# Performance work log

Measured on AMD Instinct MI355X. Metric: run time of the kernel, lower is better.

The kernel has to match this reference:

```python
import jax, jax.numpy as jnp
import numpy as np

N = 4096      # mesh nodes (seq len)
D = 512       # input_dim_nodes / hidden_size
F = 512       # ffn_hidden_size (hidden_dim)
NH = 4        # num_attention_heads
HD = D // NH  # head dim = 128
L = 2         # processor_layers
EPS = 1e-5
SCALE = 1.0 / float(np.sqrt(HD))
NEG = -1e9


def setup_inputs() -> dict:
    key = jax.random.key(0)
    ks = jax.random.split(key, 16)
    nfeat = jax.random.normal(ks[0], (N, D), jnp.float32)
    # sparse graph adjacency mask: True = masked out (TE 'arbitrary' convention)
    mask = jax.random.uniform(ks[1], (N, N)) < 0.99
    idx = jnp.arange(N)
    mask = mask.at[idx, idx].set(False)  # keep self-edges unmasked
    s = 0.02
    p = lambda k, shape: jax.random.normal(k, shape, jnp.float32) * s
    return dict(
        nfeat=nfeat, mask=mask,
        ln1_g=jnp.ones((L, D), jnp.float32), ln1_b=jnp.zeros((L, D), jnp.float32),
        wq=p(ks[2], (L, D, D)), bq=p(ks[3], (L, D)),
        wk=p(ks[4], (L, D, D)), bk=p(ks[5], (L, D)),
        wv=p(ks[6], (L, D, D)), bv=p(ks[7], (L, D)),
        wo=p(ks[8], (L, D, D)), bo=p(ks[9], (L, D)),
        ln2_g=jnp.ones((L, D), jnp.float32), ln2_b=jnp.zeros((L, D), jnp.float32),
        fc1_w=p(ks[10], (L, F, D)), fc1_b=p(ks[11], (L, F)),
        fc2_w=p(ks[12], (L, D, F)), fc2_b=p(ks[13], (L, D)),
    )


def _ln(x, g, b):
    mu = x.mean(-1, keepdims=True)
    var = ((x - mu) ** 2).mean(-1, keepdims=True)
    return (x - mu) * jax.lax.rsqrt(var + EPS) * g + b


def reference(nfeat, mask, ln1_g, ln1_b, wq, bq, wk, bk, wv, bv, wo, bo,
              ln2_g, ln2_b, fc1_w, fc1_b, fc2_w, fc2_b):
    def layer(x, p):
        g1, b1, Wq, Bq, Wk, Bk, Wv, Bv, Wo, Bo, g2, b2, W1, B1, W2, B2 = p
        # --- pre-LN self-attention with arbitrary mask ---
        h = _ln(x, g1, b1)                                  # [N, D]
        q = (h @ Wq.T + Bq).reshape(N, NH, HD)
        k = (h @ Wk.T + Bk).reshape(N, NH, HD)
        v = (h @ Wv.T + Bv).reshape(N, NH, HD)
        scores = jnp.einsum('qhd,khd->hqk', q, k) * SCALE   # [NH, N, N]
        scores = jnp.where(mask[None], NEG, scores)
        attn = jax.nn.softmax(scores, axis=-1)
        o = jnp.einsum('hqk,khd->qhd', attn, v).reshape(N, D)
        x = x + o @ Wo.T + Bo
        # --- pre-LN MLP ---
        h2 = _ln(x, g2, b2)
        m = jax.nn.gelu(h2 @ W1.T + B1, approximate=False) @ W2.T + B2
        return x + m, None

    xs = (ln1_g, ln1_b, wq, bq, wk, bk, wv, bv, wo, bo,
          ln2_g, ln2_b, fc1_w, fc1_b, fc2_w, fc2_b)
    out, _ = jax.lax.scan(layer, nfeat, xs)
    return out
```

## Files before the change

### kernel.cpp

```cpp
#include <hip/hip_runtime.h>
#include <math.h>

#define NN 4096
#define DD 512
#define FF 512
#define CAP 256
#define SCALE 0.08838834764831845f

typedef unsigned short u16;
typedef unsigned char u8;
typedef unsigned int u32;
typedef __attribute__((ext_vector_type(8))) short short8;
typedef __attribute__((ext_vector_type(8))) unsigned short ushort8;
typedef __attribute__((ext_vector_type(4))) unsigned short ushort4v;
typedef __attribute__((ext_vector_type(4))) float floatx4;
typedef __attribute__((ext_vector_type(2))) float f32x2;
typedef _Float16 half8v __attribute__((ext_vector_type(8)));

__device__ __forceinline__ u16 f2bf(float f) {
    union { float f; unsigned int i; } x; x.f = f;
    unsigned int r = (x.i + 0x7FFFu + ((x.i >> 16) & 1u)) >> 16;
    return (u16)r;
}
__device__ __forceinline__ u16 f2h(float f) {
    _Float16 h = (_Float16)f;
    union { _Float16 h; u16 u; } x; x.h = h; return x.u;
}
__device__ __forceinline__ u8 f2fp8(float f) {
    union { _Float16 h; u16 u; } x;
    x.h = (_Float16)(f * 0.00390625f);
    u16 h = x.u;
    h = h + 0x3F + ((h >> 7) & 1);
    return (u8)(((h >> 8) & 0x80) | ((h >> 7) & 0x7f));
}
__device__ __forceinline__ float fp82f_sw(u8 b) {
    union { u16 u; _Float16 h; } x;
    x.u = (u16)(((u16)(b & 0x80) << 8) | ((u16)(b & 0x7f) << 7));
    return (float)x.h * 256.0f;
}
__device__ __forceinline__ void gld_lds16(const void* g, void* l) {
    __builtin_amdgcn_global_load_lds((const __attribute__((address_space(1))) void*)g,
                                     (__attribute__((address_space(3))) void*)l, 16, 0, 0);
}

__device__ __forceinline__ float gelu_fast(float val) {
    float z = fabsf(val) * 0.70710678118654752f;
    float tt = __builtin_amdgcn_rcpf(fmaf(0.3275911f, z, 1.0f));
    float p = fmaf(1.061405429f, tt, -1.453152027f);
    p = fmaf(p, tt, 1.421413741f);
    p = fmaf(p, tt, -0.284496736f);
    p = fmaf(p, tt, 0.254829592f);
    p = p * tt * __expf(-z * z);
    float er_ = 1.0f - p;
    float sgn = (val < 0.f) ? -er_ : er_;
    return val * 0.5f * (1.0f + sgn);
}

struct SP {
    const float* w[6];
    const float* bq; const float* bk; const float* bv; const float* fc1_b;
    const float* ln1_g; const float* ln1_b; const float* ln2_g; const float* ln2_b;
    const float* nfeat; const int* mask;
};
__global__ void setup_kernel(SP sp, u16* __restrict__ wc, float* __restrict__ bc2,
                             float* __restrict__ c1c, float* __restrict__ st,
                             u16* __restrict__ xb, int* __restrict__ idx,
                             int* __restrict__ cnt) {
    const int bid = blockIdx.x;
    const int t = threadIdx.x;
    const int wave = t >> 6, lane = t & 63;
    if (bid < 192) {
        int region = bid >> 4;
        int layer = region / 6, mat = region - layer * 6;
        const float* src = sp.w[mat] + (size_t)layer * (DD * DD);
        u16* d = wc + (size_t)region * (DD * DD);
        int off = (bid & 15) * 16384 + t * 4;
        int k = (t * 4) & 511;
        float4 g4 = {1.f, 1.f, 1.f, 1.f};
        if (mat < 3)      g4 = *(const float4*)&sp.ln1_g[layer * DD + k];
        else if (mat == 4) g4 = *(const float4*)&sp.ln2_g[layer * DD + k];
#pragma unroll
        for (int i = 0; i < 16; i++) {
            int e = off + i * 1024;
            float4 f = *(const float4*)&src[e];
            ushort4v u;
            u.x = f2bf(f.x * g4.x); u.y = f2bf(f.y * g4.y);
            u.z = f2bf(f.z * g4.z); u.w = f2bf(f.w * g4.w);
            *(ushort4v*)&d[e] = u;
        }
        if (bid == 2 || bid == 3) {
            float* z = st + 8192;
            int base = (bid - 2) * 256 + t;
#pragma unroll
            for (int i = 0; i < 48; i++) z[base + i * 512] = 0.0f;
        }
        return;
    }
    if (bid < 192 + NN) {
        int row = bid - 192;
        __shared__ int c;
        __shared__ float ws[4][2];
        const float* xr = sp.nfeat + (size_t)row * DD;
        float2 v2 = *(const float2*)&xr[t * 2];
        float s1 = v2.x + v2.y, s2 = v2.x * v2.x + v2.y * v2.y;
#pragma unroll
        for (int off = 32; off; off >>= 1) { s1 += __shfl_xor(s1, off); s2 += __shfl_xor(s2, off); }
        if (lane == 0) { ws[wave][0] = s1; ws[wave][1] = s2; }
        u32 pack = (u32)f2bf(v2.x) | ((u32)f2bf(v2.y) << 16);
        ((u32*)xb)[row * 256 + t] = pack;
        if (t == 0) c = 0;
        __syncthreads();
        if (t == 0) {
            float S1 = ws[0][0] + ws[1][0] + ws[2][0] + ws[3][0];
            float S2 = ws[0][1] + ws[1][1] + ws[2][1] + ws[3][1];
            st[row * 2] = S1; st[row * 2 + 1] = S2;
        }
        const int4* mrow = (const int4*)(sp.mask + (size_t)row * NN);
        for (int j4 = t; j4 < NN / 4; j4 += blockDim.x) {
            int4 m4 = mrow[j4];
            int base = j4 * 4;
            if (m4.x == 0) idx[row * CAP + atomicAdd(&c, 1)] = base;
            if (m4.y == 0) idx[row * CAP + atomicAdd(&c, 1)] = base + 1;
            if (m4.z == 0) idx[row * CAP + atomicAdd(&c, 1)] = base + 2;
            if (m4.w == 0) idx[row * CAP + atomicAdd(&c, 1)] = base + 3;
        }
        __syncthreads();
        if (t == 0) cnt[row] = (c < CAP) ? c : CAP;
        return;
    }
    {
        int colg = (bid - (192 + NN)) * 4 + wave;
        int l = colg >> 11, j = colg & 2047;
        const float* W; const float* g; const float* b; float bias;
        if (j < 1536) {
            int mat = j >> 9, col = j & 511;
            W = sp.w[mat] + (size_t)l * DD * DD + (size_t)col * DD;
            g = sp.ln1_g + l * DD; b = sp.ln1_b + l * DD;
            bias = (mat == 0 ? sp.bq : mat == 1 ? sp.bk : sp.bv)[l * DD + col];
        } else {
            int col = j - 1536;
            W = sp.w[4] + (size_t)l * DD * DD + (size_t)col * DD;
            g = sp.ln2_g + l * DD; b = sp.ln2_b + l * DD;
            bias = sp.fc1_b[l * DD + col];
        }
        int k = lane * 8;
        float4 w0 = *(const float4*)&W[k];
        float4 w1 = *(const float4*)&W[k + 4];
        float4 g0 = *(const float4*)&g[k];
        float4 g1 = *(const float4*)&g[k + 4];
        float4 b0 = *(const float4*)&b[k];
        float4 b1 = *(const float4*)&b[k + 4];
        float c1 = w0.x * g0.x + w0.y * g0.y + w0.z * g0.z + w0.w * g0.w
                 + w1.x * g1.x + w1.y * g1.y + w1.z * g1.z + w1.w * g1.w;
        float c2 = w0.x * b0.x + w0.y * b0.y + w0.z * b0.z + w0.w * b0.w
                 + w1.x * b1.x + w1.y * b1.y + w1.z * b1.z + w1.w * b1.w;
#pragma unroll
        for (int off = 32; off; off >>= 1) { c1 += __shfl_xor(c1, off); c2 += __shfl_xor(c2, off); }
        if (lane == 0) { c1c[colg] = c1; bc2[colg] = bias + c2; }
    }
}


template <int MODE, int LNF>
__launch_bounds__(256)
__global__ void gemm_fc(const u16* __restrict__ A, const u16* __restrict__ B,
                        const float* __restrict__ bias, const float* __restrict__ c1,
                        const float* __restrict__ stats, const float* __restrict__ resIn,
                        float* __restrict__ resOut, u16* __restrict__ outB,
                        u16* __restrict__ xbOut, float* __restrict__ statsOut) {
    __shared__ __align__(16) u8 smem[16384];
    u16* As = (u16*)smem;
    u16* Bs = (u16*)(smem + 8192);
    const int m0 = blockIdx.y * 64, n0 = blockIdx.x * 64;
    const int t = threadIdx.x;
    const int wave = t >> 6, lane = t & 63;
    const int wm = (wave & 1) * 32, wn = (wave >> 1) * 32;
    const int sr = t >> 3;
    const int sc = ((((t & 7) - (t >> 3)) & 7)) * 8;
    const int fr = lane & 15, g0 = lane >> 4;
    const int er = (lane >> 4) * 4, ec = lane & 15;

    floatx4 acc[2][2] = {};
    const u16* ag0 = A + (size_t)(m0 + sr) * 512 + sc;
    const u16* ag1 = A + (size_t)(m0 + 32 + sr) * 512 + sc;
    const u16* bg0 = B + (size_t)(n0 + sr) * 512 + sc;
    const u16* bg1 = B + (size_t)(n0 + 32 + sr) * 512 + sc;

    float rin[16];
    if (MODE == 2) {
#pragma unroll
        for (int i = 0; i < 2; i++)
#pragma unroll
            for (int j = 0; j < 2; j++)
#pragma unroll
                for (int r = 0; r < 4; r++)
                    rin[(i * 2 + j) * 4 + r] =
                        resIn[(size_t)(m0 + wm + 16 * i + er + r) * 512 + (n0 + wn + 16 * j + ec)];
    }
    float ar[2][4], br[2][4];
    if (LNF) {
#pragma unroll
        for (int i = 0; i < 2; i++) {
            int r0 = m0 + wm + 16 * i + er;
#pragma unroll
            for (int r = 0; r < 4; r++) {
                f32x2 s = *(const f32x2*)&stats[(r0 + r) * 2];
                float m = s.x * (1.0f / DD);
                float rr = rsqrtf(s.y * (1.0f / DD) - m * m + 1e-5f);
                ar[i][r] = rr; br[i][r] = -rr * m;
            }
        }
    }

    for (int k0 = 0; k0 < 512; k0 += 64) {
        __syncthreads();
        gld_lds16(ag0 + k0, As + t * 8);
        gld_lds16(ag1 + k0, As + 2048 + t * 8);
        gld_lds16(bg0 + k0, Bs + t * 8);
        gld_lds16(bg1 + k0, Bs + 2048 + t * 8);
        __syncthreads();
#pragma unroll
        for (int h = 0; h < 2; h++) {
            const int fo = (((h << 2) + g0 + fr) & 7) << 3;
            short8 af[2], bf[2];
#pragma unroll
            for (int i = 0; i < 2; i++) af[i] = *(const short8*)&As[(wm + 16 * i + fr) * 64 + fo];
#pragma unroll
            for (int j = 0; j < 2; j++) bf[j] = *(const short8*)&Bs[(wn + 16 * j + fr) * 64 + fo];
#pragma unroll
            for (int i = 0; i < 2; i++)
#pragma unroll
                for (int j = 0; j < 2; j++)
                    acc[i][j] = __builtin_amdgcn_mfma_f32_16x16x32_bf16(af[i], bf[j], acc[i][j], 0, 0, 0);
        }
    }

    float outv[16];
#pragma unroll
    for (int j = 0; j < 2; j++) {
        int col = n0 + wn + 16 * j + ec;
        float bsv = bias[col];
        float c1v = LNF ? c1[col] : 0.f;
#pragma unroll
        for (int i = 0; i < 2; i++) {
#pragma unroll
            for (int r = 0; r < 4; r++) {
                int row = m0 + wm + 16 * i + er + r;
                float val;
                if (LNF) val = fmaf(ar[i][r], acc[i][j][r], fmaf(br[i][r], c1v, bsv));
                else     val = acc[i][j][r] + bsv;
                if (MODE == 1) {
                    outB[(size_t)row * 512 + col] = f2bf(gelu_fast(val));
                } else {
                    float ov = rin[(i * 2 + j) * 4 + r] + val;
                    outv[(i * 2 + j) * 4 + r] = ov;
                    resOut[(size_t)row * 512 + col] = ov;
                    if (xbOut) xbOut[(size_t)row * 512 + col] = f2bf(ov);
                }
            }
        }
    }

    if (MODE == 2 && statsOut) {
        __syncthreads();
        float* Ls = (float*)smem;
#pragma unroll
        for (int i = 0; i < 2; i++)
#pragma unroll
            for (int j = 0; j < 2; j++)
#pragma unroll
                for (int r = 0; r < 4; r++)
                    Ls[(wm + 16 * i + er + r) * 64 + (wn + 16 * j + ec)] = outv[(i * 2 + j) * 4 + r];
        __syncthreads();
        if (t < 64) {
            float s1 = 0.f, s2 = 0.f;
            for (int c0 = 0; c0 < 64; c0++) {
                int cc = (c0 + t) & 63;
                float v = Ls[t * 64 + cc];
                s1 += v; s2 += v * v;
            }
            atomicAdd(&statsOut[(size_t)(m0 + t) * 2], s1);
            atomicAdd(&statsOut[(size_t)(m0 + t) * 2 + 1], s2);
        }
    }
}

__launch_bounds__(256)
__global__ void gemm_qkv(const u16* __restrict__ A, const u16* __restrict__ B,
                         const float* __restrict__ bias, const float* __restrict__ c1,
                         const float* __restrict__ stats, u16* __restrict__ qOut,
                         u8* __restrict__ kv8) {
    __shared__ u16 As[128 * 64];
    __shared__ u16 Bs[64 * 64];
    const int m0 = blockIdx.y * 128, n0 = blockIdx.x * 64;
    const int t = threadIdx.x;
    const int wave = t >> 6, lane = t & 63;
    const int wm = (wave & 1) * 64, wn = (wave >> 1) * 32;
    const int sr = t >> 3;
    const int sc = ((((t & 7) - (t >> 3)) & 7)) * 8;
    const int fr = lane & 15, g0 = lane >> 4;
    const int er = (lane >> 4) * 4, ec = lane & 15;

    floatx4 acc[4][2] = {};
    const u16* agp[4];
    u16* asp[4];
#pragma unroll
    for (int u = 0; u < 4; u++) {
        agp[u] = A + (size_t)(m0 + 32 * u + sr) * DD + sc;
        asp[u] = As + u * (32 * 64) + t * 8;
    }
    const u16* bg0 = B + (size_t)(n0 + sr) * DD + sc;
    const u16* bg1 = B + (size_t)(n0 + 32 + sr) * DD + sc;

    float ar[4][4], br[4][4];
#pragma unroll
    for (int i = 0; i < 4; i++) {
        int r0 = m0 + wm + 16 * i + er;
#pragma unroll
        for (int r = 0; r < 4; r++) {
            f32x2 s = *(const f32x2*)&stats[(r0 + r) * 2];
            float m = s.x * (1.0f / DD);
            float rr = rsqrtf(s.y * (1.0f / DD) - m * m + 1e-5f);
            ar[i][r] = rr; br[i][r] = -rr * m;
        }
    }

    for (int k0 = 0; k0 < DD; k0 += 64) {
        __syncthreads();
#pragma unroll
        for (int u = 0; u < 4; u++) gld_lds16(agp[u] + k0, asp[u]);
        gld_lds16(bg0 + k0, Bs + t * 8);
        gld_lds16(bg1 + k0, Bs + 2048 + t * 8);
        __syncthreads();
#pragma unroll
        for (int h = 0; h < 2; h++) {
            const int fo = (((h << 2) + g0 + fr) & 7) << 3;
            short8 af[4], bf[2];
#pragma unroll
            for (int i = 0; i < 4; i++) af[i] = *(const short8*)&As[(wm + 16 * i + fr) * 64 + fo];
#pragma unroll
            for (int j = 0; j < 2; j++) bf[j] = *(const short8*)&Bs[(wn + 16 * j + fr) * 64 + fo];
#pragma unroll
            for (int i = 0; i < 4; i++)
#pragma unroll
                for (int j = 0; j < 2; j++)
                    acc[i][j] = __builtin_amdgcn_mfma_f32_16x16x32_bf16(af[i], bf[j], acc[i][j], 0, 0, 0);
        }
    }

    const int bx = blockIdx.x;
#pragma unroll
    for (int j = 0; j < 2; j++) {
        int col = n0 + wn + 16 * j + ec;
        float bsv = bias[col];
        float c1v = c1[col];
#pragma unroll
        for (int i = 0; i < 4; i++) {
#pragma unroll
            for (int r = 0; r < 4; r++) {
                int row = m0 + wm + 16 * i + er + r;
                float val = fmaf(ar[i][r], acc[i][j][r], fmaf(br[i][r], c1v, bsv));
                if (bx < 8) {
                    qOut[(size_t)row * 512 + col] = f2h(val);
                } else if (bx < 16) {
                    int cc = col - 512;
                    kv8[(size_t)row * 1024 + 16 * (cc >> 3) + (cc & 7)] = f2fp8(val);
                } else {
                    int cc = col - 1024;
                    kv8[(size_t)row * 1024 + 16 * (cc >> 3) + 8 + (cc & 7)] = f2fp8(val);
                }
            }
        }
    }
}

__global__ void sparse_attn(const u16* __restrict__ q, const u8* __restrict__ kv8,
                            const int* __restrict__ idx, const int* __restrict__ cnt,
                            u16* __restrict__ o) {
    int t = threadIdx.x;
    int wave = t >> 6, lane = t & 63;
    int qslot = wave >> 1, half = wave & 1;
    int qi = blockIdx.x * 4 + qslot;
    __shared__ float obuf[4][64][8];
    __shared__ float sbuf[4][64];
    __shared__ int sidx[4][CAP];

    int c = cnt[qi];
    const int* ir = idx + qi * CAP;
    for (int j = t & 127; j < c; j += 128) sidx[qslot][j] = ir[j];

    half8v qv = *(const half8v*)(q + (size_t)qi * 512 + lane * 8);
    float qf[8];
#pragma unroll
    for (int e = 0; e < 8; e++) qf[e] = (float)qv[e];
    __syncthreads();

    float sum = 0.f, oa[8] = {};
    int j = half;
    int4 kv0, kv1;
    {
        int k0i = (j < c) ? sidx[qslot][j] : 0;
        int k1i = (j + 2 < c) ? sidx[qslot][j + 2] : 0;
        kv0 = *(const int4*)(kv8 + (size_t)k0i * 1024 + lane * 16);
        kv1 = *(const int4*)(kv8 + (size_t)k1i * 1024 + lane * 16);
    }
    while (j < c) {
        int4 kvn;
        {
            int kjn = (j + 4 < c) ? sidx[qslot][j + 4] : 0;
            kvn = *(const int4*)(kv8 + (size_t)kjn * 1024 + lane * 16);
        }
        float kd[8], vd[8];
#if __has_builtin(__builtin_amdgcn_cvt_pk_f32_fp8)
        {
            f32x2 p0 = __builtin_amdgcn_cvt_pk_f32_fp8(kv0.x, false);
            f32x2 p1 = __builtin_amdgcn_cvt_pk_f32_fp8(kv0.x, true);
            f32x2 p2 = __builtin_amdgcn_cvt_pk_f32_fp8(kv0.y, false);
            f32x2 p3 = __builtin_amdgcn_cvt_pk_f32_fp8(kv0.y, true);
            kd[0] = p0.x; kd[1] = p0.y; kd[2] = p1.x; kd[3] = p1.y;
            kd[4] = p2.x; kd[5] = p2.y; kd[6] = p3.x; kd[7] = p3.y;
            f32x2 p4 = __builtin_amdgcn_cvt_pk_f32_fp8(kv0.z, false);
            f32x2 p5 = __builtin_amdgcn_cvt_pk_f32_fp8(kv0.z, true);
            f32x2 p6 = __builtin_amdgcn_cvt_pk_f32_fp8(kv0.w, false);
            f32x2 p7 = __builtin_amdgcn_cvt_pk_f32_fp8(kv0.w, true);
            vd[0] = p4.x; vd[1] = p4.y; vd[2] = p5.x; vd[3] = p5.y;
            vd[4] = p6.x; vd[5] = p6.y; vd[6] = p7.x; vd[7] = p7.y;
        }
#else
        {
            const u8* bp = (const u8*)&kv0;
#pragma unroll
            for (int e = 0; e < 8; e++) { kd[e] = fp82f_sw(bp[e]); vd[e] = fp82f_sw(bp[8 + e]); }
        }
#endif
        float d = 0.f;
#pragma unroll
        for (int e = 0; e < 8; e++) d = fmaf(qf[e], kd[e], d);
        d += __shfl_xor(d, 1);
        d += __shfl_xor(d, 2);
        d += __shfl_xor(d, 4);
        d += __shfl_xor(d, 8);
        float p = __expf(d * SCALE);
        sum += p;
#pragma unroll
        for (int e = 0; e < 8; e++) oa[e] = fmaf(p, vd[e], oa[e]);
        kv0 = kv1;
        kv1 = kvn;
        j += 2;
    }

    if (half == 1) {
#pragma unroll
        for (int e = 0; e < 8; e++) obuf[qslot][lane][e] = oa[e];
        sbuf[qslot][lane] = sum;
    }
    __syncthreads();
    if (half == 0) {
        sum += sbuf[qslot][lane];
        float inv = 1.0f / sum;
        ushort8 ov;
#pragma unroll
        for (int e = 0; e < 8; e++) ov[e] = f2bf((oa[e] + obuf[qslot][lane][e]) * inv);
        *(ushort8*)(o + (size_t)qi * 512 + lane * 8) = ov;
    }
}

extern "C" void kernel_launch(void* const* d_in, const int* in_sizes, int n_in,
                              void* d_out, int out_size, void* d_ws, size_t ws_size,
                              hipStream_t stream) {
    const float* nfeat = (const float*)d_in[0];
    const float* bo    = (const float*)d_in[11];
    const float* fc2_b = (const float*)d_in[17];

    const size_t ND = (size_t)NN * DD;
    const size_t SS = (size_t)DD * DD;
    float* x    = (float*)d_ws;
    u16*   xb   = (u16*)(x + ND);
    u16*   q    = xb + ND;
    u8*    kv8  = (u8*)(q + ND);
    u16*   o    = (u16*)(kv8 + (size_t)NN * 1024);
    u16*   m1   = o + ND;
    u16*   wc   = m1 + ND;
    float* bc2  = (float*)(wc + 12 * SS);
    float* c1c  = bc2 + 2 * 2048;
    float* st   = c1c + 2 * 2048;
    int*   idx  = (int*)(st + 4 * 8192);
    int*   cnt  = idx + (size_t)NN * CAP;

    SP sp;
    sp.w[0] = (const float*)d_in[4];  sp.bq = (const float*)d_in[5];
    sp.w[1] = (const float*)d_in[6];  sp.bk = (const float*)d_in[7];
    sp.w[2] = (const float*)d_in[8];  sp.bv = (const float*)d_in[9];
    sp.w[3] = (const float*)d_in[10];
    sp.w[4] = (const float*)d_in[14]; sp.fc1_b = (const float*)d_in[15];
    sp.w[5] = (const float*)d_in[16];
    sp.ln1_g = (const float*)d_in[2];  sp.ln1_b = (const float*)d_in[3];
    sp.ln2_g = (const float*)d_in[12]; sp.ln2_b = (const float*)d_in[13];
    sp.nfeat = nfeat; sp.mask = (const int*)d_in[1];

    setup_kernel<<<192 + NN + 1024, 256, 0, stream>>>(sp, wc, bc2, c1c, st, xb, idx, cnt);

    for (int l = 0; l < 2; l++) {
        size_t bOff = (size_t)l * DD;
        u16* wl = wc + (size_t)l * 6 * SS;
        const float* xin = (l == 0) ? nfeat : x;
        float* fc2_dst = (l == 1) ? (float*)d_out : x;
        float* st_ln1 = st + (l == 0 ? 0 : 2) * 8192;
        float* st_ln2 = st + (l == 0 ? 1 : 3) * 8192;

        gemm_qkv<<<dim3(24, 32), 256, 0, stream>>>(xb, wl, bc2 + l * 2048, c1c + l * 2048,
                                                   st_ln1, q, kv8);
        sparse_attn<<<NN / 4, 512, 0, stream>>>(q, kv8, idx, cnt, o);
        gemm_fc<2, 0><<<dim3(8, 64), 256, 0, stream>>>(o, wl + 3 * SS, bo + bOff, nullptr,
                                                       nullptr, xin, x, nullptr, xb, st_ln2);
        gemm_fc<1, 1><<<dim3(8, 64), 256, 0, stream>>>(xb, wl + 4 * SS,
                                                       bc2 + l * 2048 + 1536,
                                                       c1c + l * 2048 + 1536,
                                                       st_ln2, nullptr, nullptr, m1,
                                                       nullptr, nullptr);
        gemm_fc<2, 0><<<dim3(8, 64), 256, 0, stream>>>(m1, wl + 5 * SS, fc2_b + bOff, nullptr,
                                                       nullptr, x, fc2_dst, nullptr,
                                                       (l == 0) ? xb : nullptr,
                                                       (l == 0) ? (st + 2 * 8192) : nullptr);
    }
}
```

Before: 272.7 us.

## Move mask compaction into layer-0 QKV GEMM using wave ballot prefix sums

The sparse-mask index compaction leaves the setup kernel and runs in extra blocks appended to the layer-0 QKV GEMM grid, so the mask scan overlaps with the GEMM work. Each wave now compacts one row in order using ballot and popcount instead of shared-memory atomics. This also yields deterministic, sorted neighbour lists. The setup kernel's per-row LN statistics and bf16 conversion are reshaped to one row per wave, which cuts the setup grid. The cost is a larger QKV launch with heterogeneous blocks, and the mask read (64 MB of int32) still dominates and now sits on the QKV kernel's critical path.

```diff
diff --git a/kernel.cpp b/kernel.cpp
--- a/kernel.cpp
+++ b/kernel.cpp
@@ -60,12 +60,11 @@
     const float* w[6];
     const float* bq; const float* bk; const float* bv; const float* fc1_b;
     const float* ln1_g; const float* ln1_b; const float* ln2_g; const float* ln2_b;
-    const float* nfeat; const int* mask;
+    const float* nfeat;
 };
 __global__ void setup_kernel(SP sp, u16* __restrict__ wc, float* __restrict__ bc2,
                              float* __restrict__ c1c, float* __restrict__ st,
-                             u16* __restrict__ xb, int* __restrict__ idx,
-                             int* __restrict__ cnt) {
+                             u16* __restrict__ xb) {
     const int bid = blockIdx.x;
     const int t = threadIdx.x;
     const int wave = t >> 6, lane = t & 63;
@@ -96,40 +95,26 @@
         }
         return;
     }
-    if (bid < 192 + NN) {
-        int row = bid - 192;
-        __shared__ int c;
-        __shared__ float ws[4][2];
-        const float* xr = sp.nfeat + (size_t)row * DD;
-        float2 v2 = *(const float2*)&xr[t * 2];
-        float s1 = v2.x + v2.y, s2 = v2.x * v2.x + v2.y * v2.y;
+    if (bid < 192 + 1024) {
+        int row = (bid - 192) * 4 + wave;
+        const float* xr = sp.nfeat + (size_t)row * DD + lane * 8;
+        float4 a = *(const float4*)xr;
+        float4 b4 = *(const float4*)(xr + 4);
+        float v[8] = {a.x, a.y, a.z, a.w, b4.x, b4.y, b4.z, b4.w};
+        float s1 = 0.f, s2 = 0.f;
+#pragma unroll
+        for (int e = 0; e < 8; e++) { s1 += v[e]; s2 += v[e] * v[e]; }
 #pragma unroll
         for (int off = 32; off; off >>= 1) { s1 += __shfl_xor(s1, off); s2 += __shfl_xor(s2, off); }
-        if (lane == 0) { ws[wave][0] = s1; ws[wave][1] = s2; }
-        u32 pack = (u32)f2bf(v2.x) | ((u32)f2bf(v2.y) << 16);
-        ((u32*)xb)[row * 256 + t] = pack;
-        if (t == 0) c = 0;
-        __syncthreads();
-        if (t == 0) {
-            float S1 = ws[0][0] + ws[1][0] + ws[2][0] + ws[3][0];
-            float S2 = ws[0][1] + ws[1][1] + ws[2][1] + ws[3][1];
-            st[row * 2] = S1; st[row * 2 + 1] = S2;
-        }
-        const int4* mrow = (const int4*)(sp.mask + (size_t)row * NN);
-        for (int j4 = t; j4 < NN / 4; j4 += blockDim.x) {
-            int4 m4 = mrow[j4];
-            int base = j4 * 4;
-            if (m4.x == 0) idx[row * CAP + atomicAdd(&c, 1)] = base;
-            if (m4.y == 0) idx[row * CAP + atomicAdd(&c, 1)] = base + 1;
-            if (m4.z == 0) idx[row * CAP + atomicAdd(&c, 1)] = base + 2;
-            if (m4.w == 0) idx[row * CAP + atomicAdd(&c, 1)] = base + 3;
-        }
-        __syncthreads();
-        if (t == 0) cnt[row] = (c < CAP) ? c : CAP;
+        if (lane == 0) { st[row * 2] = s1; st[row * 2 + 1] = s2; }
+        ushort8 ov;
+#pragma unroll
+        for (int e = 0; e < 8; e++) ov[e] = f2bf(v[e]);
+        *(ushort8*)&xb[(size_t)row * DD + lane * 8] = ov;
         return;
     }
     {
-        int colg = (bid - (192 + NN)) * 4 + wave;
+        int colg = (bid - (192 + 1024)) * 4 + wave;
         int l = colg >> 11, j = colg & 2047;
         const float* W; const float* g; const float* b; float bias;
         if (j < 1536) {
@@ -285,16 +270,44 @@
     }
 }
 
+template <int DOMASK>
 __launch_bounds__(256)
 __global__ void gemm_qkv(const u16* __restrict__ A, const u16* __restrict__ B,
                          const float* __restrict__ bias, const float* __restrict__ c1,
                          const float* __restrict__ stats, u16* __restrict__ qOut,
-                         u8* __restrict__ kv8) {
+                         u8* __restrict__ kv8, const int* __restrict__ mask,
+                         int* __restrict__ idx, int* __restrict__ cnt) {
     __shared__ u16 As[128 * 64];
     __shared__ u16 Bs[64 * 64];
-    const int m0 = blockIdx.y * 128, n0 = blockIdx.x * 64;
     const int t = threadIdx.x;
     const int wave = t >> 6, lane = t & 63;
+
+    if (DOMASK && blockIdx.y >= 32) {
+        int mb = (blockIdx.y - 32) * 24 + blockIdx.x;
+        int row = mb * 4 + wave;
+        if (row < NN) {
+            const int4* mrow = (const int4*)(mask + (size_t)row * NN);
+            int base = 0;
+#pragma unroll 4
+            for (int it = 0; it < 16; it++) {
+                int4 m4 = mrow[it * 64 + lane];
+                int cbase = (it * 64 + lane) * 4;
+                int mv[4] = {m4.x, m4.y, m4.z, m4.w};
+#pragma unroll
+                for (int cmp = 0; cmp < 4; cmp++) {
+                    unsigned long long bl = __ballot(mv[cmp] == 0);
+                    int pre = __popcll(bl & ((1ull << lane) - 1ull));
+                    int pos = base + pre;
+                    if (mv[cmp] == 0 && pos < CAP) idx[row * CAP + pos] = cbase + cmp;
+                    base += __popcll(bl);
+                }
+            }
+            if (lane == 0) cnt[row] = (base < CAP) ? base : CAP;
+        }
+        return;
+    }
+
+    const int m0 = blockIdx.y * 128, n0 = blockIdx.x * 64;
     const int wm = (wave & 1) * 64, wn = (wave >> 1) * 32;
     const int sr = t >> 3;
     const int sc = ((((t & 7) - (t >> 3)) & 7)) * 8;
@@ -469,6 +482,7 @@
                               void* d_out, int out_size, void* d_ws, size_t ws_size,
                               hipStream_t stream) {
     const float* nfeat = (const float*)d_in[0];
+    const int*   mask  = (const int*)d_in[1];
     const float* bo    = (const float*)d_in[11];
     const float* fc2_b = (const float*)d_in[17];
 
@@ -496,9 +510,9 @@
     sp.w[5] = (const float*)d_in[16];
     sp.ln1_g = (const float*)d_in[2];  sp.ln1_b = (const float*)d_in[3];
     sp.ln2_g = (const float*)d_in[12]; sp.ln2_b = (const float*)d_in[13];
-    sp.nfeat = nfeat; sp.mask = (const int*)d_in[1];
-
-    setup_kernel<<<192 + NN + 1024, 256, 0, stream>>>(sp, wc, bc2, c1c, st, xb, idx, cnt);
+    sp.nfeat = nfeat;
+
+    setup_kernel<<<192 + 1024 + 1024, 256, 0, stream>>>(sp, wc, bc2, c1c, st, xb);
 
     for (int l = 0; l < 2; l++) {
         size_t bOff = (size_t)l * DD;
@@ -508,8 +522,13 @@
         float* st_ln1 = st + (l == 0 ? 0 : 2) * 8192;
         float* st_ln2 = st + (l == 0 ? 1 : 3) * 8192;
 
-        gemm_qkv<<<dim3(24, 32), 256, 0, stream>>>(xb, wl, bc2 + l * 2048, c1c + l * 2048,
-                                                   st_ln1, q, kv8);
+        if (l == 0) {
+            gemm_qkv<1><<<dim3(24, 32 + 43), 256, 0, stream>>>(xb, wl, bc2, c1c,
+                                                               st_ln1, q, kv8, mask, idx, cnt);
+        } else {
+            gemm_qkv<0><<<dim3(24, 32), 256, 0, stream>>>(xb, wl, bc2 + 2048, c1c + 2048,
+                                                          st_ln1, q, kv8, nullptr, idx, cnt);
+        }
         sparse_attn<<<NN / 4, 512, 0, stream>>>(q, kv8, idx, cnt, o);
         gemm_fc<2, 0><<<dim3(8, 64), 256, 0, stream>>>(o, wl + 3 * SS, bo + bOff, nullptr,
                                                        nullptr, xin, x, nullptr, xb, st_ln2);
```

Result: slower. 280.9 us (+3.0%).
